# Kernel tuning notes

Hardware: AMD Instinct MI355X
Metric: run time of the kernel (lower is better)

The kernel has to match this reference:

```python
import jax, jax.numpy as jnp
import numpy as np

WS = 8          # window side -> N = 64
DIM = 512
NH = 16
B_ = 1024       # batch * num_windows
CPB_HIDDEN = 512


def _make_coords_table():
    # relative_coords_table: (1, 2*WS-1, 2*WS-1, 2), log-spaced continuous coords
    r = np.arange(-(WS - 1), WS, dtype=np.float32)
    t = np.stack(np.meshgrid(r, r, indexing='ij'), axis=-1)[None]  # (1,15,15,2)
    t = t / (WS - 1)
    t = t * 8.0
    t = np.sign(t) * np.log2(np.abs(t) + 1.0) / np.log2(8.0)
    return t.astype(np.float32)


def _make_rel_pos_index():
    coords = np.stack(np.meshgrid(np.arange(WS), np.arange(WS), indexing='ij'))  # (2,WS,WS)
    cf = coords.reshape(2, -1)                       # (2, N)
    rel = (cf[:, :, None] - cf[:, None, :]).transpose(1, 2, 0).astype(np.int64)  # (N,N,2)
    rel[..., 0] += WS - 1
    rel[..., 1] += WS - 1
    rel[..., 0] *= 2 * WS - 1
    return rel.sum(-1)  # (N, N) int


def setup_inputs() -> dict:
    key = jax.random.key(0)
    ks = jax.random.split(key, 10)
    s_in = 1.0 / np.sqrt(DIM)
    inp = {
        'x': jax.random.normal(ks[0], (B_, WS * WS, DIM), dtype=jnp.float32),
        'qkv_weight': jax.random.normal(ks[1], (3 * DIM, DIM), dtype=jnp.float32) * s_in,
        'q_bias': jnp.zeros((DIM,), dtype=jnp.float32),
        'v_bias': jnp.zeros((DIM,), dtype=jnp.float32),
        'logit_scale': jnp.full((NH, 1, 1), np.log(10.0), dtype=jnp.float32),
        'cpb_w1': jax.random.normal(ks[2], (CPB_HIDDEN, 2), dtype=jnp.float32) * (1.0 / np.sqrt(2.0)),
        'cpb_b1': jnp.zeros((CPB_HIDDEN,), dtype=jnp.float32),
        'cpb_w2': jax.random.normal(ks[3], (NH, CPB_HIDDEN), dtype=jnp.float32) * (1.0 / np.sqrt(CPB_HIDDEN)),
        'proj_w': jax.random.normal(ks[4], (DIM, DIM), dtype=jnp.float32) * s_in,
        'proj_b': jnp.zeros((DIM,), dtype=jnp.float32),
        'rel_coords_table': jnp.asarray(_make_coords_table()),
        'rel_pos_index': jnp.asarray(_make_rel_pos_index()),
    }
    return inp


def reference(x, qkv_weight, q_bias, v_bias, logit_scale, cpb_w1, cpb_b1, cpb_w2,
              proj_w, proj_b, rel_coords_table, rel_pos_index):
    B, N, C = x.shape
    nh = logit_scale.shape[0]
    hd = C // nh

    # qkv projection; bias = [q_bias, 0, v_bias] (k has no bias, Swin-V2 style)
    qkv_bias = jnp.concatenate([q_bias, jnp.zeros_like(q_bias), v_bias])
    qkv = x @ qkv_weight.T + qkv_bias                       # (B, N, 3C)
    qkv = qkv.reshape(B, N, 3, nh, hd).transpose(2, 0, 3, 1, 4)  # (3, B, nh, N, hd)
    q, k, v = qkv[0], qkv[1], qkv[2]

    # continuous position bias MLP: Linear(2,512)+ReLU -> Linear(512,nh, no bias)
    hidden = jax.nn.relu(rel_coords_table @ cpb_w1.T + cpb_b1)  # (1,15,15,512)
    table = (hidden @ cpb_w2.T).reshape(-1, nh)                 # ((2W-1)^2, nh)
    rpb = table[rel_pos_index.reshape(-1)].reshape(N, N, nh).transpose(2, 0, 1)
    rpb = 16.0 * jax.nn.sigmoid(rpb)                            # (nh, N, N)

    # fused attention math: (QK^T)*logit_scale + bias -> softmax -> AV
    scores = jnp.einsum('bhnd,bhmd->bhnm', q, k) * logit_scale.reshape(1, nh, 1, 1)
    scores = scores + rpb[None]
    attn = jax.nn.softmax(scores, axis=-1)
    out = jnp.einsum('bhnm,bhmd->bhnd', attn, v)                # (B, nh, N, hd)
    out = out.transpose(0, 2, 1, 3).reshape(B, N, C)

    return out @ proj_w.T + proj_b
```

## Files before the change

### kernel.cpp

```cpp
#include <hip/hip_runtime.h>
#include <hip/hip_bf16.h>
#include <stdint.h>
#include <stddef.h>


typedef unsigned short ushort_t;
typedef _Float16 half_t;
typedef __attribute__((ext_vector_type(8))) _Float16 half8;
typedef __attribute__((ext_vector_type(4))) float f32x4;

#define MROWS 65536

__device__ __forceinline__ ushort_t h_bits(half_t h) {
  union { half_t h; ushort_t u; } c; c.h = h; return c.u;
}

__device__ __forceinline__ void gload16(const void* g, void* l) {
  __builtin_amdgcn_global_load_lds(
      (const __attribute__((address_space(1))) unsigned int*)g,
      (__attribute__((address_space(3))) unsigned int*)l, 16, 0, 0);
}

__global__ __launch_bounds__(256) void k_split(const float* __restrict__ src,
                                               ushort_t* __restrict__ hi,
                                               ushort_t* __restrict__ lo, int n4) {
  int stride = gridDim.x * blockDim.x;
  for (int i = blockIdx.x * blockDim.x + threadIdx.x; i < n4; i += stride) {
    f32x4 x = reinterpret_cast<const f32x4*>(src)[i];
    ushort_t h4[4], l4[4];
#pragma unroll
    for (int j = 0; j < 4; ++j) {
      half_t hh = (half_t)x[j];
      h4[j] = h_bits(hh);
      l4[j] = h_bits((half_t)(x[j] - (float)hh));
    }
    reinterpret_cast<uint2*>(hi)[i] =
        make_uint2(h4[0] | ((unsigned)h4[1] << 16), h4[2] | ((unsigned)h4[3] << 16));
    reinterpret_cast<uint2*>(lo)[i] =
        make_uint2(l4[0] | ((unsigned)l4[1] << 16), l4[2] | ((unsigned)l4[3] << 16));
  }
}

__global__ __launch_bounds__(256) void k_cpb1(const float* __restrict__ coords,
                                              const float* __restrict__ w1,
                                              const float* __restrict__ b1,
                                              const float* __restrict__ w2,
                                              float* __restrict__ tbl) {
  __shared__ float hid[512];
  int p = blockIdx.x;
  float c0 = coords[2 * p], c1 = coords[2 * p + 1];
  int t = threadIdx.x;
  for (int j = t; j < 512; j += 256) {
    float v = c0 * w1[2 * j] + c1 * w1[2 * j + 1] + b1[j];
    hid[j] = v > 0.f ? v : 0.f;
  }
  __syncthreads();
  int wid = t >> 6, lane = t & 63;
#pragma unroll
  for (int hh = 0; hh < 4; ++hh) {
    int head = wid * 4 + hh;
    float s = 0.f;
    for (int j = lane; j < 512; j += 64) s += hid[j] * w2[head * 512 + j];
#pragma unroll
    for (int off = 32; off > 0; off >>= 1) s += __shfl_xor(s, off);
    if (lane == 0) tbl[p * 16 + head] = 16.f / (1.f + __expf(-s));
  }
}

__global__ __launch_bounds__(256) void k_cpb2(const float* __restrict__ tbl,
                                              const int* __restrict__ ridx,
                                              float* __restrict__ rpb) {
  int idx = blockIdx.x * 256 + threadIdx.x;
  int h = idx >> 12, nm = idx & 4095;
  rpb[idx] = tbl[ridx[nm] * 16 + h];
}

__global__ __launch_bounds__(256, 2) void k_qkv(
    const ushort_t* __restrict__ Wh, const ushort_t* __restrict__ Wl,
    const float* __restrict__ X,
    const float* __restrict__ qb, const float* __restrict__ vb,
    ushort_t* __restrict__ oqh, ushort_t* __restrict__ oql,
    ushort_t* __restrict__ okh, ushort_t* __restrict__ okl,
    ushort_t* __restrict__ ovt) {
  __shared__ ushort_t lAh[2][4096];
  __shared__ ushort_t lAl[2][4096];
  __shared__ ushort_t lBh[2][4096];
  __shared__ ushort_t lBl[2][4096];

  int nwg = gridDim.x, bid = blockIdx.x;
  int idx = ((nwg & 7) == 0) ? ((bid & 7) * (nwg >> 3) + (bid >> 3)) : bid;
  int tm = idx % 12, tn = idx / 12;
  int tid = threadIdx.x;
  int wid = tid >> 6, lane = tid & 63;
  int wr = wid >> 1, wc = wid & 1;
  int lr = lane & 15, lq = lane >> 4;

  int rA = tid >> 2, qA = tid & 3;
  size_t gA = (size_t)(tm * 128 + rA) * 512 + ((qA ^ (rA & 3)) << 3);
  int dA = wid * 512;

  int rB = tid >> 3, qB = tid & 7;
  const float* gB = X + (size_t)(tn * 128 + rB) * 512 + qB * 4;
  int dB = rB * 32 + (((qB >> 1) ^ (rB & 3)) << 3) + ((qB & 1) << 2);

  f32x4 acc[4][4];
#pragma unroll
  for (int i = 0; i < 4; ++i)
#pragma unroll
    for (int j = 0; j < 4; ++j)
#pragma unroll
      for (int r = 0; r < 4; ++r) acc[i][j][r] = 0.f;

  auto stageA = [&](int kk, int bs) {
    gload16(Wh + gA + kk, &lAh[bs][dA]);
    gload16(Wh + gA + 32768 + kk, &lAh[bs][2048 + dA]);
    gload16(Wl + gA + kk, &lAl[bs][dA]);
    gload16(Wl + gA + 32768 + kk, &lAl[bs][2048 + dA]);
  };
  auto loadB = [&](int kk, f32x4* xr) {
#pragma unroll
    for (int s = 0; s < 4; ++s) xr[s] = *(const f32x4*)(gB + s * 16384 + kk);
  };
  auto writeB = [&](const f32x4* xr, int bs) {
#pragma unroll
    for (int s = 0; s < 4; ++s) {
      ushort_t h4[4], l4[4];
#pragma unroll
      for (int e = 0; e < 4; ++e) {
        half_t hh = (half_t)xr[s][e];
        h4[e] = h_bits(hh);
        l4[e] = h_bits((half_t)(xr[s][e] - (float)hh));
      }
      *(uint2*)&lBh[bs][dB + s * 1024] =
          make_uint2(h4[0] | ((unsigned)h4[1] << 16), h4[2] | ((unsigned)h4[3] << 16));
      *(uint2*)&lBl[bs][dB + s * 1024] =
          make_uint2(l4[0] | ((unsigned)l4[1] << 16), l4[2] | ((unsigned)l4[3] << 16));
    }
  };

  f32x4 xr[4];
  stageA(0, 0);
  loadB(0, xr);
  writeB(xr, 0);
  const int c16 = (lq ^ (lr & 3)) << 3;
#pragma unroll 2
  for (int t = 0; t < 16; ++t) {
    __syncthreads();
    int bs = t & 1;
    if (t < 15) {
      stageA((t + 1) * 32, bs ^ 1);
      loadB((t + 1) * 32, xr);
    }
    half8 ah[4], al[4], bh[4], bl[4];
#pragma unroll
    for (int i = 0; i < 4; ++i) {
      int ro = (wr * 64 + i * 16 + lr) * 32 + c16;
      ah[i] = *(const half8*)&lAh[bs][ro];
      al[i] = *(const half8*)&lAl[bs][ro];
    }
#pragma unroll
    for (int j = 0; j < 4; ++j) {
      int ro = (wc * 64 + j * 16 + lr) * 32 + c16;
      bh[j] = *(const half8*)&lBh[bs][ro];
      bl[j] = *(const half8*)&lBl[bs][ro];
    }
#pragma unroll
    for (int i = 0; i < 4; ++i)
#pragma unroll
      for (int j = 0; j < 4; ++j) {
        acc[i][j] = __builtin_amdgcn_mfma_f32_16x16x32_f16(ah[i], bh[j], acc[i][j], 0, 0, 0);
        acc[i][j] = __builtin_amdgcn_mfma_f32_16x16x32_f16(ah[i], bl[j], acc[i][j], 0, 0, 0);
        acc[i][j] = __builtin_amdgcn_mfma_f32_16x16x32_f16(al[i], bh[j], acc[i][j], 0, 0, 0);
      }
    if (t < 15) writeB(xr, bs ^ 1);
  }

#pragma unroll
  for (int i = 0; i < 4; ++i) {
    int ch0 = tm * 128 + wr * 64 + i * 16 + lq * 4;
#pragma unroll
    for (int j = 0; j < 4; ++j) {
      int tok = tn * 128 + wc * 64 + j * 16 + lr;
      int sec = tm >> 2;
      int h = (ch0 >> 5) & 15, d0 = ch0 & 31;
      int win = tok >> 6, n = tok & 63;
      size_t pr = (size_t)win * 16 + h;
      f32x4 b4;
      if (sec == 0)      b4 = *(const f32x4*)&qb[ch0];
      else if (sec == 2) b4 = *(const f32x4*)&vb[ch0 - 1024];
      else { b4[0] = 0.f; b4[1] = 0.f; b4[2] = 0.f; b4[3] = 0.f; }
      if (sec == 2) {
#pragma unroll
        for (int r = 0; r < 4; ++r) {
          float v = acc[i][j][r] + b4[r];
          ovt[(pr * 32 + d0 + r) * 64 + n] = h_bits((half_t)v);
        }
      } else {
        ushort_t hb[4], lb4[4];
#pragma unroll
        for (int r = 0; r < 4; ++r) {
          float v = acc[i][j][r] + b4[r];
          half_t hh = (half_t)v;
          hb[r] = h_bits(hh);
          lb4[r] = h_bits((half_t)(v - (float)hh));
        }
        uint2 hw = make_uint2(hb[0] | ((unsigned)hb[1] << 16), hb[2] | ((unsigned)hb[3] << 16));
        uint2 lw = make_uint2(lb4[0] | ((unsigned)lb4[1] << 16), lb4[2] | ((unsigned)lb4[3] << 16));
        size_t o = (pr * 64 + n) * 32 + d0;
        if (sec == 0) { *(uint2*)&oqh[o] = hw; *(uint2*)&oql[o] = lw; }
        else          { *(uint2*)&okh[o] = hw; *(uint2*)&okl[o] = lw; }
      }
    }
  }
}

__global__ __launch_bounds__(256, 2) void k_proj(
    const ushort_t* __restrict__ Wh, const ushort_t* __restrict__ Wl,
    const ushort_t* __restrict__ Bp,
    const float* __restrict__ pb, float* __restrict__ outp) {
  __shared__ ushort_t lAh[2][4096];
  __shared__ ushort_t lAl[2][4096];
  __shared__ ushort_t lBh[2][4096];

  int nwg = gridDim.x, bid = blockIdx.x;
  int idx = ((nwg & 7) == 0) ? ((bid & 7) * (nwg >> 3) + (bid >> 3)) : bid;
  int tm = idx % 4, tn = idx / 4;
  int tid = threadIdx.x;
  int wid = tid >> 6, lane = tid & 63;
  int wr = wid >> 1, wc = wid & 1;
  int lr = lane & 15, lq = lane >> 4;

  int rA = tid >> 2, qA = tid & 3;
  int sw = (qA ^ (rA & 3)) << 3;
  size_t gA = (size_t)(tm * 128 + rA) * 512 + sw;
  size_t gB = (size_t)(tn * 128 + rA) * 512 + sw;
  int dA = wid * 512;

  f32x4 acc[4][4];
#pragma unroll
  for (int i = 0; i < 4; ++i)
#pragma unroll
    for (int j = 0; j < 4; ++j)
#pragma unroll
      for (int r = 0; r < 4; ++r) acc[i][j][r] = 0.f;

  auto stage = [&](int kk, int bs) {
    gload16(Wh + gA + kk, &lAh[bs][dA]);
    gload16(Wh + gA + 32768 + kk, &lAh[bs][2048 + dA]);
    gload16(Wl + gA + kk, &lAl[bs][dA]);
    gload16(Wl + gA + 32768 + kk, &lAl[bs][2048 + dA]);
    gload16(Bp + gB + kk, &lBh[bs][dA]);
    gload16(Bp + gB + 32768 + kk, &lBh[bs][2048 + dA]);
  };

  stage(0, 0);
  const int c16 = (lq ^ (lr & 3)) << 3;
#pragma unroll 2
  for (int t = 0; t < 16; ++t) {
    __syncthreads();
    int bs = t & 1;
    if (t < 15) stage((t + 1) * 32, bs ^ 1);
    half8 ah[4], al[4], bh[4];
#pragma unroll
    for (int i = 0; i < 4; ++i) {
      int ro = (wr * 64 + i * 16 + lr) * 32 + c16;
      ah[i] = *(const half8*)&lAh[bs][ro];
      al[i] = *(const half8*)&lAl[bs][ro];
    }
#pragma unroll
    for (int j = 0; j < 4; ++j)
      bh[j] = *(const half8*)&lBh[bs][(wc * 64 + j * 16 + lr) * 32 + c16];
#pragma unroll
    for (int i = 0; i < 4; ++i)
#pragma unroll
      for (int j = 0; j < 4; ++j) {
        acc[i][j] = __builtin_amdgcn_mfma_f32_16x16x32_f16(ah[i], bh[j], acc[i][j], 0, 0, 0);
        acc[i][j] = __builtin_amdgcn_mfma_f32_16x16x32_f16(al[i], bh[j], acc[i][j], 0, 0, 0);
      }
  }

#pragma unroll
  for (int i = 0; i < 4; ++i) {
    int ch0 = tm * 128 + wr * 64 + i * 16 + lq * 4;
    f32x4 b4 = *(const f32x4*)&pb[ch0];
#pragma unroll
    for (int j = 0; j < 4; ++j) {
      int tok = tn * 128 + wc * 64 + j * 16 + lr;
      f32x4 o;
#pragma unroll
      for (int r = 0; r < 4; ++r) o[r] = acc[i][j][r] + b4[r];
      *(f32x4*)&outp[(size_t)tok * 512 + ch0] = o;
    }
  }
}

__global__ __launch_bounds__(128) void k_attn(
    const ushort_t* __restrict__ qph, const ushort_t* __restrict__ qpl,
    const ushort_t* __restrict__ kph, const ushort_t* __restrict__ kpl,
    const ushort_t* __restrict__ vt,
    const float* __restrict__ rpb, const float* __restrict__ lsc,
    ushort_t* __restrict__ oh) {
  __shared__ unsigned pw[2][2][64 * 36];
  const int tid = threadIdx.x;
  const int wid = tid >> 6, lane = tid & 63;
  const int pair = blockIdx.x * 2 + wid;
  const int h = pair & 15;
  const int l15 = lane & 15, lq = lane >> 4;
  const size_t base = (size_t)pair * 2048;

  half8 Kh[4], Kl[4], Qh[4], Ql[4];
#pragma unroll
  for (int t4 = 0; t4 < 4; ++t4) {
    int off = (t4 * 16 + l15) * 32 + lq * 8;
    Kh[t4] = *(const half8*)(kph + base + off);
    Kl[t4] = *(const half8*)(kpl + base + off);
    Qh[t4] = *(const half8*)(qph + base + off);
    Ql[t4] = *(const half8*)(qpl + base + off);
  }
  f32x4 st[4][4];
#pragma unroll
  for (int a = 0; a < 4; ++a)
#pragma unroll
    for (int b = 0; b < 4; ++b)
#pragma unroll
      for (int r = 0; r < 4; ++r) st[a][b][r] = 0.f;
#pragma unroll
  for (int kvt = 0; kvt < 4; ++kvt)
#pragma unroll
    for (int qt = 0; qt < 4; ++qt) {
      st[kvt][qt] = __builtin_amdgcn_mfma_f32_16x16x32_f16(Kh[kvt], Qh[qt], st[kvt][qt], 0, 0, 0);
      st[kvt][qt] = __builtin_amdgcn_mfma_f32_16x16x32_f16(Kh[kvt], Ql[qt], st[kvt][qt], 0, 0, 0);
      st[kvt][qt] = __builtin_amdgcn_mfma_f32_16x16x32_f16(Kl[kvt], Qh[qt], st[kvt][qt], 0, 0, 0);
    }

  const float ls = lsc[h];
  const float* rb = rpb + ((size_t)h << 12);
  float mx[4], sm[4], inv[4];
#pragma unroll
  for (int qt = 0; qt < 4; ++qt) {
    int qg = qt * 16 + l15;
    mx[qt] = -1e30f;
#pragma unroll
    for (int kvt = 0; kvt < 4; ++kvt) {
      f32x4 r4 = *(const f32x4*)(rb + qg * 64 + kvt * 16 + lq * 4);
#pragma unroll
      for (int r = 0; r < 4; ++r) {
        float z = st[kvt][qt][r] * ls + r4[r];
        st[kvt][qt][r] = z;
        mx[qt] = fmaxf(mx[qt], z);
      }
    }
    mx[qt] = fmaxf(mx[qt], __shfl_xor(mx[qt], 16));
    mx[qt] = fmaxf(mx[qt], __shfl_xor(mx[qt], 32));
    sm[qt] = 0.f;
#pragma unroll
    for (int kvt = 0; kvt < 4; ++kvt)
#pragma unroll
      for (int r = 0; r < 4; ++r) {
        float e = __expf(st[kvt][qt][r] - mx[qt]);
        st[kvt][qt][r] = e;
        sm[qt] += e;
      }
    sm[qt] += __shfl_xor(sm[qt], 16);
    sm[qt] += __shfl_xor(sm[qt], 32);
    inv[qt] = 1.f / sm[qt];
  }

#pragma unroll
  for (int qt = 0; qt < 4; ++qt) {
    int qg = qt * 16 + l15;
#pragma unroll
    for (int kvt = 0; kvt < 4; ++kvt)
#pragma unroll
      for (int p2 = 0; p2 < 2; ++p2) {
        float pa = st[kvt][qt][2 * p2] * inv[qt];
        float pc = st[kvt][qt][2 * p2 + 1] * inv[qt];
        half_t ha = (half_t)pa, hc = (half_t)pc;
        unsigned wh = h_bits(ha) | ((unsigned)h_bits(hc) << 16);
        unsigned wl = h_bits((half_t)(pa - (float)ha)) |
                      ((unsigned)h_bits((half_t)(pc - (float)hc)) << 16);
        int kv = kvt * 16 + lq * 4 + 2 * p2;
        pw[wid][0][qg * 36 + (kv >> 1)] = wh;
        pw[wid][1][qg * 36 + (kv >> 1)] = wl;
      }
  }

  half8 Vf[2][2];
#pragma unroll
  for (int dt = 0; dt < 2; ++dt)
#pragma unroll
    for (int ks = 0; ks < 2; ++ks)
      Vf[dt][ks] = *(const half8*)(vt + base + (dt * 16 + l15) * 64 + ks * 32 + lq * 8);
  f32x4 ot[2][4];
#pragma unroll
  for (int a = 0; a < 2; ++a)
#pragma unroll
    for (int b = 0; b < 4; ++b)
#pragma unroll
      for (int r = 0; r < 4; ++r) ot[a][b][r] = 0.f;
  const char* pb0 = (const char*)&pw[wid][0][0];
  const char* pb1 = (const char*)&pw[wid][1][0];
#pragma unroll
  for (int qt = 0; qt < 4; ++qt)
#pragma unroll
    for (int ks = 0; ks < 2; ++ks) {
      int off = (qt * 16 + l15) * 144 + ks * 64 + lq * 16;
      half8 Pf = *(const half8*)(pb0 + off);
      half8 Pl = *(const half8*)(pb1 + off);
#pragma unroll
      for (int dt = 0; dt < 2; ++dt) {
        ot[dt][qt] = __builtin_amdgcn_mfma_f32_16x16x32_f16(Vf[dt][ks], Pf, ot[dt][qt], 0, 0, 0);
        ot[dt][qt] = __builtin_amdgcn_mfma_f32_16x16x32_f16(Vf[dt][ks], Pl, ot[dt][qt], 0, 0, 0);
      }
    }

  int win = pair >> 4;
#pragma unroll
  for (int dt = 0; dt < 2; ++dt)
#pragma unroll
    for (int qt = 0; qt < 4; ++qt) {
      int t = win * 64 + qt * 16 + l15;
      int d0 = dt * 16 + lq * 4;
      ushort_t hb[4];
#pragma unroll
      for (int r = 0; r < 4; ++r) hb[r] = h_bits((half_t)ot[dt][qt][r]);
      *(uint2*)&oh[(size_t)t * 512 + h * 32 + d0] =
          make_uint2(hb[0] | ((unsigned)hb[1] << 16), hb[2] | ((unsigned)hb[3] << 16));
    }
}

extern "C" void kernel_launch(void* const* d_in, const int* in_sizes, int n_in,
                              void* d_out, int out_size, void* d_ws, size_t ws_size,
                              hipStream_t stream) {
  const float* x      = (const float*)d_in[0];
  const float* qkvw   = (const float*)d_in[1];
  const float* qb     = (const float*)d_in[2];
  const float* vb     = (const float*)d_in[3];
  const float* lsc    = (const float*)d_in[4];
  const float* w1     = (const float*)d_in[5];
  const float* b1     = (const float*)d_in[6];
  const float* w2     = (const float*)d_in[7];
  const float* pwt    = (const float*)d_in[8];
  const float* pb     = (const float*)d_in[9];
  const float* coords = (const float*)d_in[10];
  const int*   ridx   = (const int*)d_in[11];
  float* out = (float*)d_out;
  char* ws = (char*)d_ws;

  size_t off = 0;
  auto alloc = [&](size_t bytes) {
    size_t r = off;
    off = (off + bytes + 255) & ~(size_t)255;
    return r;
  };
  size_t oWQH = alloc((size_t)1536 * 512 * 2);
  size_t oWQL = alloc((size_t)1536 * 512 * 2);
  size_t oWPH = alloc((size_t)512 * 512 * 2);
  size_t oWPL = alloc((size_t)512 * 512 * 2);
  size_t oRPB = alloc((size_t)16 * 4096 * 4);
  size_t oTBL = alloc((size_t)225 * 16 * 4);
  size_t fixed = off;

  int S = 1;
  while (S <= 32) {
    size_t Ms = (size_t)MROWS / S;
    size_t need = fixed + Ms * 1024 * 6 + 4096;
    if (need <= ws_size) break;
    S <<= 1;
  }
  if (S > 64) S = 64;
  size_t Ms = (size_t)MROWS / S;

  size_t oQH = alloc(Ms * 1024);
  size_t oQL = alloc(Ms * 1024);
  size_t oKH = alloc(Ms * 1024);
  size_t oKL = alloc(Ms * 1024);
  size_t oVT = alloc(Ms * 1024);
  size_t oAO = alloc(Ms * 1024);

  ushort_t* wqh = (ushort_t*)(ws + oWQH);
  ushort_t* wql = (ushort_t*)(ws + oWQL);
  ushort_t* wph = (ushort_t*)(ws + oWPH);
  ushort_t* wpl = (ushort_t*)(ws + oWPL);
  float* rpb = (float*)(ws + oRPB);
  float* tbl = (float*)(ws + oTBL);
  ushort_t* qh = (ushort_t*)(ws + oQH);
  ushort_t* ql = (ushort_t*)(ws + oQL);
  ushort_t* kh = (ushort_t*)(ws + oKH);
  ushort_t* kl = (ushort_t*)(ws + oKL);
  ushort_t* vt = (ushort_t*)(ws + oVT);
  ushort_t* ao = (ushort_t*)(ws + oAO);

  k_split<<<768, 256, 0, stream>>>(qkvw, wqh, wql, 1536 * 512 / 4);
  k_split<<<256, 256, 0, stream>>>(pwt, wph, wpl, 512 * 512 / 4);
  k_cpb1<<<225, 256, 0, stream>>>(coords, w1, b1, w2, tbl);
  k_cpb2<<<256, 256, 0, stream>>>(tbl, ridx, rpb);

  int ntn = (int)(Ms / 128);
  int g0 = 12 * ntn;
  int g1 = 4 * ntn;
  int ga = (int)((Ms / 64) * 16 / 2);

  for (int s = 0; s < S; ++s) {
    const float* xs = x + (size_t)s * Ms * 512;
    k_qkv<<<g0, 256, 0, stream>>>(wqh, wql, xs, qb, vb, qh, ql, kh, kl, vt);
    k_attn<<<ga, 128, 0, stream>>>(qh, ql, kh, kl, vt, rpb, lsc, ao);
    k_proj<<<g1, 256, 0, stream>>>(wph, wpl, ao, pb, out + (size_t)s * Ms * 512);
  }
  (void)in_sizes; (void)n_in; (void)out_size; (void)ws_size;
}
```

Before: 843.9 us.

## Load X directly into registers for MFMA and widen QKV tile to 256 tokens

The QKV GEMM no longer stages the activation tile through LDS. Each lane reads its fp32 X fragment straight from global memory, splits it into fp16 hi/lo in registers, and feeds the MFMA directly. The token tile per workgroup doubles to 256, so each wave holds 4x8 accumulators and the grid halves. This removes the LDS writes, reads and half the shared memory, but it raises register pressure, reads global memory with a strided per-lane pattern, and drops the software-pipelined prefetch of B.

```diff
diff --git a/kernel.cpp b/kernel.cpp
--- a/kernel.cpp
+++ b/kernel.cpp
@@ -84,8 +84,6 @@
     ushort_t* __restrict__ ovt) {
   __shared__ ushort_t lAh[2][4096];
   __shared__ ushort_t lAl[2][4096];
-  __shared__ ushort_t lBh[2][4096];
-  __shared__ ushort_t lBl[2][4096];
 
   int nwg = gridDim.x, bid = blockIdx.x;
   int idx = ((nwg & 7) == 0) ? ((bid & 7) * (nwg >> 3) + (bid >> 3)) : bid;
@@ -99,15 +97,13 @@
   size_t gA = (size_t)(tm * 128 + rA) * 512 + ((qA ^ (rA & 3)) << 3);
   int dA = wid * 512;
 
-  int rB = tid >> 3, qB = tid & 7;
-  const float* gB = X + (size_t)(tn * 128 + rB) * 512 + qB * 4;
-  int dB = rB * 32 + (((qB >> 1) ^ (rB & 3)) << 3) + ((qB & 1) << 2);
-
-  f32x4 acc[4][4];
+  const float* xb = X + (size_t)(tn * 256 + wc * 128 + lr) * 512 + lq * 8;
+
+  f32x4 acc[4][8];
 #pragma unroll
   for (int i = 0; i < 4; ++i)
 #pragma unroll
-    for (int j = 0; j < 4; ++j)
+    for (int j = 0; j < 8; ++j)
 #pragma unroll
       for (int r = 0; r < 4; ++r) acc[i][j][r] = 0.f;
 
@@ -117,70 +113,62 @@
     gload16(Wl + gA + kk, &lAl[bs][dA]);
     gload16(Wl + gA + 32768 + kk, &lAl[bs][2048 + dA]);
   };
-  auto loadB = [&](int kk, f32x4* xr) {
-#pragma unroll
-    for (int s = 0; s < 4; ++s) xr[s] = *(const f32x4*)(gB + s * 16384 + kk);
-  };
-  auto writeB = [&](const f32x4* xr, int bs) {
-#pragma unroll
-    for (int s = 0; s < 4; ++s) {
-      ushort_t h4[4], l4[4];
-#pragma unroll
-      for (int e = 0; e < 4; ++e) {
-        half_t hh = (half_t)xr[s][e];
-        h4[e] = h_bits(hh);
-        l4[e] = h_bits((half_t)(xr[s][e] - (float)hh));
-      }
-      *(uint2*)&lBh[bs][dB + s * 1024] =
-          make_uint2(h4[0] | ((unsigned)h4[1] << 16), h4[2] | ((unsigned)h4[3] << 16));
-      *(uint2*)&lBl[bs][dB + s * 1024] =
-          make_uint2(l4[0] | ((unsigned)l4[1] << 16), l4[2] | ((unsigned)l4[3] << 16));
-    }
-  };
-
-  f32x4 xr[4];
+
   stageA(0, 0);
-  loadB(0, xr);
-  writeB(xr, 0);
   const int c16 = (lq ^ (lr & 3)) << 3;
 #pragma unroll 2
   for (int t = 0; t < 16; ++t) {
     __syncthreads();
-    int bs = t & 1;
-    if (t < 15) {
-      stageA((t + 1) * 32, bs ^ 1);
-      loadB((t + 1) * 32, xr);
-    }
-    half8 ah[4], al[4], bh[4], bl[4];
+    int bs = t & 1, kk = t * 32;
+    if (t < 15) stageA(kk + 32, bs ^ 1);
+
+    f32x4 x0a = *(const f32x4*)(xb + kk);
+    f32x4 x0b = *(const f32x4*)(xb + kk + 4);
+    f32x4 x1a = *(const f32x4*)(xb + 8192 + kk);
+    f32x4 x1b = *(const f32x4*)(xb + 8192 + kk + 4);
+
+    half8 ah[4], al[4];
 #pragma unroll
     for (int i = 0; i < 4; ++i) {
       int ro = (wr * 64 + i * 16 + lr) * 32 + c16;
       ah[i] = *(const half8*)&lAh[bs][ro];
       al[i] = *(const half8*)&lAl[bs][ro];
     }
-#pragma unroll
-    for (int j = 0; j < 4; ++j) {
-      int ro = (wc * 64 + j * 16 + lr) * 32 + c16;
-      bh[j] = *(const half8*)&lBh[bs][ro];
-      bl[j] = *(const half8*)&lBl[bs][ro];
-    }
-#pragma unroll
-    for (int i = 0; i < 4; ++i)
-#pragma unroll
-      for (int j = 0; j < 4; ++j) {
-        acc[i][j] = __builtin_amdgcn_mfma_f32_16x16x32_f16(ah[i], bh[j], acc[i][j], 0, 0, 0);
-        acc[i][j] = __builtin_amdgcn_mfma_f32_16x16x32_f16(ah[i], bl[j], acc[i][j], 0, 0, 0);
-        acc[i][j] = __builtin_amdgcn_mfma_f32_16x16x32_f16(al[i], bh[j], acc[i][j], 0, 0, 0);
-      }
-    if (t < 15) writeB(xr, bs ^ 1);
+
+#pragma unroll
+    for (int j = 0; j < 8; ++j) {
+      f32x4 ca = (j & 1) ? x1a : x0a;
+      f32x4 cb = (j & 1) ? x1b : x0b;
+      if (j < 6) {
+        const float* p = xb + (size_t)(j + 2) * 8192 + kk;
+        if (j & 1) { x1a = *(const f32x4*)p; x1b = *(const f32x4*)(p + 4); }
+        else       { x0a = *(const f32x4*)p; x0b = *(const f32x4*)(p + 4); }
+      }
+      half8 bh, bl;
+#pragma unroll
+      for (int e = 0; e < 4; ++e) {
+        half_t h0 = (half_t)ca[e];
+        bh[e] = h0;
+        bl[e] = (half_t)(ca[e] - (float)h0);
+        half_t h1 = (half_t)cb[e];
+        bh[4 + e] = h1;
+        bl[4 + e] = (half_t)(cb[e] - (float)h1);
+      }
+#pragma unroll
+      for (int i = 0; i < 4; ++i) {
+        acc[i][j] = __builtin_amdgcn_mfma_f32_16x16x32_f16(ah[i], bh, acc[i][j], 0, 0, 0);
+        acc[i][j] = __builtin_amdgcn_mfma_f32_16x16x32_f16(ah[i], bl, acc[i][j], 0, 0, 0);
+        acc[i][j] = __builtin_amdgcn_mfma_f32_16x16x32_f16(al[i], bh, acc[i][j], 0, 0, 0);
+      }
+    }
   }
 
 #pragma unroll
   for (int i = 0; i < 4; ++i) {
     int ch0 = tm * 128 + wr * 64 + i * 16 + lq * 4;
 #pragma unroll
-    for (int j = 0; j < 4; ++j) {
-      int tok = tn * 128 + wc * 64 + j * 16 + lr;
+    for (int j = 0; j < 8; ++j) {
+      int tok = tn * 256 + wc * 128 + j * 16 + lr;
       int sec = tm >> 2;
       int h = (ch0 >> 5) & 15, d0 = ch0 & 31;
       int win = tok >> 6, n = tok & 63;
@@ -496,8 +484,9 @@
   k_cpb1<<<225, 256, 0, stream>>>(coords, w1, b1, w2, tbl);
   k_cpb2<<<256, 256, 0, stream>>>(tbl, ridx, rpb);
 
+  int ntn256 = (int)(Ms / 256);
+  int g0 = 12 * ntn256;
   int ntn = (int)(Ms / 128);
-  int g0 = 12 * ntn;
   int g1 = 4 * ntn;
   int ga = (int)((Ms / 64) * 16 / 2);
 
```

Measured after the change: 991.9 us. 1.18x slower.
